# Performance work log

Hardware: AMD Instinct MI355X
Metric: run time of the kernel (lower is better)

## Reference

```python
import jax, jax.numpy as jnp
import numpy as np

L, B, I, H = 256, 16, 2048, 2048
S = R = T = 32  # s_size == t_size is required by the read-hop chaining


def setup_inputs() -> dict:
    key = jax.random.key(0)
    ks = jax.random.split(key, 8)
    def p(k, shape, scale=0.02):
        return jax.random.normal(k, shape, jnp.float32) * scale
    return dict(
        inputs=jax.random.normal(ks[0], (L, B, I), jnp.float32),
        h0=jnp.zeros((B, H), jnp.float32),
        c0=jnp.zeros((B, H), jnp.float32),
        F0=jnp.zeros((B, S * R, T), jnp.float32),
        W_ih=p(ks[1], (4 * H, I)),
        W_hh=p(ks[2], (4 * H, H)),
        b_ih=jnp.zeros((4 * H,), jnp.float32),
        b_hh=jnp.zeros((4 * H,), jnp.float32),
        Ww_w=p(ks[3], (S + R + T + 1, H)),
        Ww_b=jnp.zeros((S + R + T + 1,), jnp.float32),
        Wr_w=p(ks[4], (S + 3 * R, H)),
        Wr_b=jnp.zeros((S + 3 * R,), jnp.float32),
        Wlin_w=p(ks[5], (H, T)),
        Wlin_b=jnp.zeros((H,), jnp.float32),
    )


def _ln(x, eps=1e-5):
    # LayerNorm without affine params (elementwise_affine=False)
    m = jnp.mean(x, -1, keepdims=True)
    v = jnp.var(x, -1, keepdims=True)
    return (x - m) * jax.lax.rsqrt(v + eps)


def reference(inputs, h0, c0, F0, W_ih, W_hh, b_ih, b_hh,
              Ww_w, Ww_b, Wr_w, Wr_b, Wlin_w, Wlin_b):
    # ---- single-layer LSTM (PyTorch gate order i,f,g,o) ----
    bias = b_ih + b_hh
    def lstm_step(carry, x_t):
        h, c = carry
        g = x_t @ W_ih.T + h @ W_hh.T + bias            # [B,4H]
        i, f, gg, o = jnp.split(g, 4, axis=-1)
        c = jax.nn.sigmoid(f) * c + jax.nn.sigmoid(i) * jnp.tanh(gg)
        h = jax.nn.sigmoid(o) * jnp.tanh(c)
        return (h, c), h
    _, x = jax.lax.scan(lstm_step, (h0, c0), inputs)     # x: [L,B,H]

    # ---- Fast Weight Memory: per-step write then 3-hop read ----
    def fwm_step(Fm, x_t):
        # write
        w = x_t @ Ww_w.T + Ww_b                          # [B, S+R+T+1]
        s = jnp.tanh(w[:, :S])
        r = jnp.tanh(w[:, S:S + R])
        t = jnp.tanh(w[:, S + R:S + R + T])
        b = jax.nn.sigmoid(w[:, S + R + T:] + 1.0)       # [B,1]
        sr = (s[:, :, None] * r[:, None, :]).reshape(-1, S * R)   # [B,S*R]
        v = jnp.einsum('bk,bkt->bt', sr, Fm)             # [B,T]
        Fm = Fm + sr[:, :, None] * (b * (t - v))[:, None, :]
        n = jnp.linalg.norm(Fm.reshape(Fm.shape[0], -1), axis=-1)
        Fm = Fm / (jax.nn.relu(n - 1.0) + 1.0)[:, None, None]
        # read (3 hops)
        rv = jnp.tanh(x_t @ Wr_w.T + Wr_b)               # [B, S+3R]
        q = rv[:, :S]
        for j in range(3):
            rj = rv[:, S + j * R:S + (j + 1) * R]
            nr = (q[:, :, None] * rj[:, None, :]).reshape(q.shape[0], -1)
            q = _ln(jnp.einsum('bk,bkt->bt', nr, Fm))    # [B,T]
        return Fm, q

    _, qs = jax.lax.scan(fwm_step, F0, x)                # qs: [L,B,T]
    return x + qs @ Wlin_w.T + Wlin_b                    # [L,B,H]
```

## Files before the change

kernel.cpp:

```cpp
#include <hip/hip_runtime.h>
#include <hip/hip_bf16.h>
#include <cstdint>
#include <cstddef>

#define L_DIM 256
#define B_DIM 16
#define I_DIM 2048
#define H_DIM 2048
#define G4    8192
#define MROWS 4096
#define NWGL  128
#define NPRJ  16
#define NSCN  16

typedef __hip_bfloat16 bf16;
typedef __bf16 bf16x8_t __attribute__((ext_vector_type(8)));
typedef _Float16 f16x8_t __attribute__((ext_vector_type(8)));
typedef _Float16 f16x4_t __attribute__((ext_vector_type(4)));
typedef float f32x4_t   __attribute__((ext_vector_type(4)));

__device__ __forceinline__ bf16 f2b(float f) { return __float2bfloat16(f); }

__device__ __forceinline__ void gl_lds16(const void* g, void* l) {
  __builtin_amdgcn_global_load_lds(
      (const __attribute__((address_space(1))) unsigned int*)g,
      (__attribute__((address_space(3))) unsigned int*)l, 16, 0, 0);
}

__device__ __forceinline__ float sigmoidf_(float x) { return 1.f / (1.f + expf(-x)); }

__device__ __forceinline__ f16x8_t load_f16x8_sc(const _Float16* p) {
  f16x8_t r;
  asm volatile("global_load_dwordx4 %0, %1, off sc0 sc1" : "=v"(r) : "v"(p));
  return r;
}
__device__ __forceinline__ bf16x8_t load_bf16x8_sc(const bf16* p) {
  bf16x8_t r;
  asm volatile("global_load_dwordx4 %0, %1, off sc0 sc1" : "=v"(r) : "v"(p));
  return r;
}
__device__ __forceinline__ float load_f32_sc(const float* p) {
  float r;
  asm volatile("global_load_dword %0, %1, off sc0 sc1" : "=v"(r) : "v"(p));
  return r;
}
__device__ __forceinline__ void store_short_sc(void* p, unsigned int v) {
  asm volatile("global_store_short %0, %1, off sc0 sc1" :: "v"(p), "v"(v) : "memory");
}
__device__ __forceinline__ void store_f32_sc(void* p, float v) {
  asm volatile("global_store_dword %0, %1, off sc0 sc1" :: "v"(p), "v"(v) : "memory");
}

__global__ void prep_kernel(const float* __restrict__ Wih, const float* __restrict__ Whh,
                            const float* __restrict__ inp, const float* __restrict__ Www,
                            const float* __restrict__ Wwb, const float* __restrict__ Wrw,
                            const float* __restrict__ h0,
                            _Float16* __restrict__ Wih_f, _Float16* __restrict__ Whh_f,
                            _Float16* __restrict__ inp_f,
                            bf16* __restrict__ Wq_hi, bf16* __restrict__ Wq_lo,
                            bf16* __restrict__ Wr_hi, bf16* __restrict__ Wr_lo,
                            float* __restrict__ wbpad,
                            _Float16* __restrict__ Xh0)
{
  size_t idx0 = (size_t)blockIdx.x * blockDim.x + threadIdx.x;
  size_t stride = (size_t)gridDim.x * blockDim.x;
  for (size_t i = idx0; i < 16777216ull; i += stride) {
    Wih_f[i] = (_Float16)Wih[i];
    Whh_f[i] = (_Float16)Whh[i];
  }
  for (size_t i = idx0; i < 8388608ull; i += stride) inp_f[i] = (_Float16)inp[i];
  for (size_t i = idx0; i < 262144ull; i += stride) {
    size_t r = i >> 11;
    float q = (r < 97) ? Www[i] : 0.f;
    bf16 qh = f2b(q);
    Wq_hi[i] = qh;
    Wq_lo[i] = f2b(q - (float)qh);
    float rr = Wrw[i];
    bf16 rh = f2b(rr);
    Wr_hi[i] = rh;
    Wr_lo[i] = f2b(rr - (float)rh);
  }
  for (size_t i = idx0; i < 128ull; i += stride) wbpad[i] = (i < 97) ? Wwb[i] : 0.f;
  for (size_t i = idx0; i < 32768ull; i += stride) Xh0[i] = (_Float16)h0[i];
}

__global__ __launch_bounds__(256) void gemm_f16(const _Float16* __restrict__ A,
                                                const _Float16* __restrict__ B,
                                                const float* __restrict__ bih,
                                                const float* __restrict__ bhh,
                                                _Float16* __restrict__ Gin2,
                                                int M, int N, int K)
{
  __shared__ __align__(16) _Float16 As[128 * 32];
  __shared__ __align__(16) _Float16 Bs[128 * 32];
  const int tid  = threadIdx.x;
  const int lane = tid & 63;
  const int w    = tid >> 6;
  const int wm   = w >> 1, wn = w & 1;
  const int m0   = blockIdx.x * 128, n0 = blockIdx.y * 128;

  f32x4_t acc[4][4];
#pragma unroll
  for (int m = 0; m < 4; ++m)
#pragma unroll
    for (int n = 0; n < 4; ++n) acc[m][n] = (f32x4_t){0.f, 0.f, 0.f, 0.f};

  for (int k0 = 0; k0 < K; k0 += 32) {
#pragma unroll
    for (int r = 0; r < 2; ++r) {
      const int base = w * 2048 + r * 1024;
      const int off  = base + lane * 16;
      const int e    = off >> 1;
      const int row  = e >> 5;
      const int col  = e & 31;
      gl_lds16(A + (size_t)(m0 + row) * K + (k0 + col), (char*)As + base);
      gl_lds16(B + (size_t)(n0 + row) * K + (k0 + col), (char*)Bs + base);
    }
    __syncthreads();

    f16x8_t af[4], bfr[4];
    const int kb = (lane >> 4) * 16;
#pragma unroll
    for (int m = 0; m < 4; ++m)
      af[m] = *reinterpret_cast<const f16x8_t*>((const char*)As + (wm * 64 + m * 16 + (lane & 15)) * 64 + kb);
#pragma unroll
    for (int n = 0; n < 4; ++n)
      bfr[n] = *reinterpret_cast<const f16x8_t*>((const char*)Bs + (wn * 64 + n * 16 + (lane & 15)) * 64 + kb);
#pragma unroll
    for (int m = 0; m < 4; ++m)
#pragma unroll
      for (int n = 0; n < 4; ++n)
        acc[m][n] = __builtin_amdgcn_mfma_f32_16x16x32_f16(af[m], bfr[n], acc[m][n], 0, 0, 0);
    __syncthreads();
  }

  const int jj = lane & 15;
#pragma unroll
  for (int n = 0; n < 4; ++n) {
    const int colb = n0 + wn * 64 + n * 16;
    const int gate = colb >> 11;
    const int wg   = (colb & 2047) >> 4;
    const float bv = bih[colb + jj] + bhh[colb + jj];
#pragma unroll
    for (int m = 0; m < 4; ++m) {
      const int rowb = m0 + wm * 64 + m * 16;
      const int t = rowb >> 4;
      f16x4_t v4;
#pragma unroll
      for (int r = 0; r < 4; ++r) v4[r] = (_Float16)(acc[m][n][r] + bv);
      *reinterpret_cast<f16x4_t*>(
          Gin2 + (((size_t)t * NWGL + wg) * 4 + gate) * 256 + jj * 16 + (lane >> 4) * 4) = v4;
    }
  }
}

__global__ __launch_bounds__(512, 2) void fused_rnn(
    const _Float16* __restrict__ Whh,
    const _Float16* __restrict__ Gin2,
    const float* __restrict__ bih, const float* __restrict__ bhh,
    const float* __restrict__ c0,
    const bf16* __restrict__ Wq_hi, const bf16* __restrict__ Wq_lo,
    const bf16* __restrict__ Wr_hi, const bf16* __restrict__ Wr_lo,
    const float* __restrict__ wbpad, const float* __restrict__ Wrb,
    const float* __restrict__ F0,
    _Float16* __restrict__ Xh,
    bf16* __restrict__ XhHi, bf16* __restrict__ XhLo,
    float* __restrict__ Wall, float* __restrict__ RVall,
    _Float16* __restrict__ Gbuf,
    int* lflags, int* pflags)
{
  __shared__ float part[8][4][16][17];
  __shared__ float s_s[32], s_r[32], s_tv[32], s_bb;
  __shared__ float s_rv[128];
  __shared__ float s_v[32];
  __shared__ float s_red[8];

  const int wgid = blockIdx.x;
  const int tid  = threadIdx.x;
  const int lane = tid & 63;
  const int wv   = tid >> 6;

  if (wgid < NWGL) {
    const int wg = wgid;
    const int j0 = wg * 16;
    const int kw = wv * 256;

    f16x8_t whh[4][8];
    {
      const int nn  = lane & 15;
      const int kfo = (lane >> 4) * 8;
#pragma unroll
      for (int g = 0; g < 4; ++g) {
        const size_t grow = (size_t)(g * H_DIM + j0 + nn) * 2048;
#pragma unroll
        for (int ks = 0; ks < 8; ++ks)
          whh[g][ks] = *reinterpret_cast<const f16x8_t*>(Whh + grow + kw + ks * 32 + kfo);
      }
    }

    float c_reg = 0.f, cbr0 = 0.f, cbr1 = 0.f, cbr2 = 0.f, cbr3 = 0.f;
    if (tid < 256) {
      const int bb = tid & 15, jj = tid >> 4;
      const int j = j0 + jj;
      c_reg = c0[bb * H_DIM + j];
      cbr0 = bih[0 * H_DIM + j] + bhh[0 * H_DIM + j];
      cbr1 = bih[1 * H_DIM + j] + bhh[1 * H_DIM + j];
      cbr2 = bih[2 * H_DIM + j] + bhh[2 * H_DIM + j];
      cbr3 = bih[3 * H_DIM + j] + bhh[3 * H_DIM + j];
    }

    const size_t arow = (size_t)(lane & 15) * 2048 + kw + (lane >> 4) * 8;
    const int fidx = ((wv << 4) + (lane & 15)) << 4;

    for (int t = 0; t < L_DIM; ++t) {
      float gin0 = 0.f, gin1 = 0.f, gin2v = 0.f, gin3 = 0.f;
      if (tid < 256) {
        const _Float16* gbase = Gin2 + ((size_t)t * NWGL + wg) * 1024;
        gin0  = (float)gbase[0 * 256 + tid];
        gin1  = (float)gbase[1 * 256 + tid];
        gin2v = (float)gbase[2 * 256 + tid];
        gin3  = (float)gbase[3 * 256 + tid];
      }

      if (t > 0) {
        while (true) {
          const int v = __hip_atomic_load(&lflags[fidx], __ATOMIC_RELAXED,
                                          __HIP_MEMORY_SCOPE_AGENT);
          if (__all(v >= t)) break;
          __builtin_amdgcn_s_sleep(1);
        }
      }

      const size_t hoff = (size_t)t * 32768 + arow;
      f16x8_t hf[8];
#pragma unroll
      for (int ks = 0; ks < 8; ++ks)
        hf[ks] = load_f16x8_sc(Xh + hoff + ks * 32);
      asm volatile("s_waitcnt vmcnt(0)" ::: "memory");
      __builtin_amdgcn_sched_barrier(0);

      f32x4_t acc[4];
#pragma unroll
      for (int g = 0; g < 4; ++g) acc[g] = (f32x4_t){0.f, 0.f, 0.f, 0.f};
#pragma unroll
      for (int ks = 0; ks < 8; ++ks) {
#pragma unroll
        for (int g = 0; g < 4; ++g)
          acc[g] = __builtin_amdgcn_mfma_f32_16x16x32_f16(hf[ks], whh[g][ks], acc[g], 0, 0, 0);
      }
#pragma unroll
      for (int g = 0; g < 4; ++g)
#pragma unroll
        for (int r = 0; r < 4; ++r)
          part[wv][g][(lane >> 4) * 4 + r][lane & 15] = acc[g][r];
      __syncthreads();

      if (tid < 256) {
        const int bb = tid & 15, jj = tid >> 4;
        float g4[4] = {gin0, gin1, gin2v, gin3};
        const float cb4[4] = {cbr0, cbr1, cbr2, cbr3};
#pragma unroll
        for (int g = 0; g < 4; ++g) {
          float s = 0.f;
#pragma unroll
          for (int v = 0; v < 8; ++v) s += part[v][g][bb][jj];
          g4[g] += s + cb4[g];
        }
        const float i_ = sigmoidf_(g4[0]);
        const float f_ = sigmoidf_(g4[1]);
        const float g_ = tanhf(g4[2]);
        const float o_ = sigmoidf_(g4[3]);
        c_reg = f_ * c_reg + i_ * g_;
        const float h = o_ * tanhf(c_reg);
        const int bj = bb * 2048 + j0 + jj;
        const _Float16 hF = (_Float16)h;
        const bf16 hhv = f2b(h);
        const bf16 hlv = f2b(h - (float)hhv);
        const size_t xi = ((size_t)t * 16 + bb) * 2048 + j0 + jj;
        store_short_sc(Xh + (size_t)(t + 1) * 32768 + bj,
                       (unsigned int)__builtin_bit_cast(unsigned short, hF));
        store_short_sc(XhHi + xi,
                       (unsigned int)__builtin_bit_cast(unsigned short, hhv));
        store_short_sc(XhLo + xi,
                       (unsigned int)__builtin_bit_cast(unsigned short, hlv));
      }
      asm volatile("s_waitcnt vmcnt(0)" ::: "memory");
      __syncthreads();

      if (tid == 0)
        __hip_atomic_store(&lflags[wg << 4], t + 1, __ATOMIC_RELAXED,
                           __HIP_MEMORY_SCOPE_AGENT);
    }

  } else if (wgid < NWGL + NPRJ) {
    const int p   = wgid - NWGL;
    const int kw  = wv * 256;
    const int nn  = lane & 15;
    const int kfo = (lane >> 4) * 8;

    bf16x8_t wbh[8], wbl[8];
    {
      const bf16* Bh = (p < 8) ? Wq_hi : Wr_hi;
      const bf16* Bl = (p < 8) ? Wq_lo : Wr_lo;
      const int brow = (p < 8) ? (p * 16 + nn) : ((p - 8) * 16 + nn);
#pragma unroll
      for (int ks = 0; ks < 8; ++ks) {
        const size_t o = (size_t)brow * 2048 + kw + ks * 32 + kfo;
        wbh[ks] = *reinterpret_cast<const bf16x8_t*>(Bh + o);
        wbl[ks] = *reinterpret_cast<const bf16x8_t*>(Bl + o);
      }
    }
    float biasv = 0.f;
    if (tid < 256) {
      const int oo = tid >> 4;
      biasv = (p < 8) ? wbpad[p * 16 + oo] : Wrb[(p - 8) * 16 + oo];
    }

    const size_t axrow = (size_t)(lane & 15) * 2048 + kw + kfo;

    for (int t = 0; t < L_DIM; ++t) {
      while (true) {
        const int v0 = __hip_atomic_load(&lflags[lane << 4], __ATOMIC_RELAXED,
                                         __HIP_MEMORY_SCOPE_AGENT);
        const int v1 = __hip_atomic_load(&lflags[(64 + lane) << 4], __ATOMIC_RELAXED,
                                         __HIP_MEMORY_SCOPE_AGENT);
        if (__all(v0 > t && v1 > t)) break;
        __builtin_amdgcn_s_sleep(1);
      }

      const size_t xoff = (size_t)t * 32768 + axrow;
      bf16x8_t xh[8], xl[8];
#pragma unroll
      for (int ks = 0; ks < 8; ++ks) {
        xh[ks] = load_bf16x8_sc(XhHi + xoff + ks * 32);
        xl[ks] = load_bf16x8_sc(XhLo + xoff + ks * 32);
      }
      asm volatile("s_waitcnt vmcnt(0)" ::: "memory");
      __builtin_amdgcn_sched_barrier(0);

      f32x4_t acc = {0.f, 0.f, 0.f, 0.f};
#pragma unroll
      for (int ks = 0; ks < 8; ++ks) {
        acc = __builtin_amdgcn_mfma_f32_16x16x32_bf16(xh[ks], wbh[ks], acc, 0, 0, 0);
        acc = __builtin_amdgcn_mfma_f32_16x16x32_bf16(xh[ks], wbl[ks], acc, 0, 0, 0);
        acc = __builtin_amdgcn_mfma_f32_16x16x32_bf16(xl[ks], wbh[ks], acc, 0, 0, 0);
      }
#pragma unroll
      for (int r = 0; r < 4; ++r)
        part[wv][0][(lane >> 4) * 4 + r][lane & 15] = acc[r];
      __syncthreads();

      if (tid < 256) {
        const int bb = tid & 15, oo = tid >> 4;
        float s = 0.f;
#pragma unroll
        for (int v = 0; v < 8; ++v) s += part[v][0][bb][oo];
        s += biasv;
        float* dst;
        if (p < 8) {
          dst = Wall + (size_t)(t * 16 + bb) * 128 + p * 16 + oo;
        } else {
          s = tanhf(s);
          dst = RVall + (size_t)(t * 16 + bb) * 128 + (p - 8) * 16 + oo;
        }
        store_f32_sc(dst, s);
      }
      asm volatile("s_waitcnt vmcnt(0)" ::: "memory");
      __syncthreads();

      if (tid == 0)
        __hip_atomic_store(&pflags[p << 4], t + 1, __ATOMIC_RELAXED,
                           __HIP_MEMORY_SCOPE_AGENT);
    }

  } else {
    const int b     = wgid - NWGL - NPRJ;
    const int si    = lane >> 1;
    const int rbase = 16 * (lane & 1);
    const int tl    = lane & 31;

    float F[16][4];
#pragma unroll
    for (int i = 0; i < 16; ++i)
#pragma unroll
      for (int j = 0; j < 4; ++j)
        F[i][j] = F0[((size_t)b * 1024 + (16 * lane + i)) * 32 + 4 * wv + j];

    float N = 0.f;
    {
      float loc = 0.f;
#pragma unroll
      for (int i = 0; i < 16; ++i)
#pragma unroll
        for (int j = 0; j < 4; ++j) loc += F[i][j] * F[i][j];
#pragma unroll
      for (int m = 1; m < 64; m <<= 1) loc += __shfl_xor(loc, m);
      if (lane == 0) s_red[wv] = loc;
      __syncthreads();
#pragma unroll
      for (int k = 0; k < 8; ++k) N += s_red[k];
    }

    for (int t = 0; t < 256; ++t) {
      while (true) {
        const int v = __hip_atomic_load(&pflags[(lane & 15) << 4], __ATOMIC_RELAXED,
                                        __HIP_MEMORY_SCOPE_AGENT);
        if (__all(v > t)) break;
        __builtin_amdgcn_s_sleep(1);
      }

      float wpre = 0.f, rvpre = 0.f;
      if (tid < 97)  wpre = load_f32_sc(Wall + (size_t)(t * 16 + b) * 128 + tid);
      if (tid >= 128 && tid < 256)
        rvpre = load_f32_sc(RVall + (size_t)(t * 16 + b) * 128 + tid - 128);
      asm volatile("s_waitcnt vmcnt(0)" ::: "memory");
      __syncthreads();
      if (tid < 32)       s_s[tid]       = tanhf(wpre);
      else if (tid < 64)  s_r[tid - 32]  = tanhf(wpre);
      else if (tid < 96)  s_tv[tid - 64] = tanhf(wpre);
      else if (tid == 96) s_bb           = sigmoidf_(wpre + 1.f);
      else if (tid >= 128 && tid < 256) s_rv[tid - 128] = rvpre;
      __syncthreads();

      const float sv = s_s[si];
      float sr[16];
#pragma unroll
      for (int i = 0; i < 16; ++i) sr[i] = sv * s_r[rbase + i];

      float vv4[4];
#pragma unroll
      for (int j = 0; j < 4; ++j) {
        float pp = 0.f;
#pragma unroll
        for (int i = 0; i < 16; ++i) pp += sr[i] * F[i][j];
#pragma unroll
        for (int m = 1; m < 64; m <<= 1) pp += __shfl_xor(pp, m);
        vv4[j] = pp;
      }
      if (lane == 0) {
#pragma unroll
        for (int j = 0; j < 4; ++j) s_v[4 * wv + j] = vv4[j];
      }
      __syncthreads();

      const float vt  = s_v[tl];
      const float ut  = s_bb * (s_tv[tl] - vt);
      const float sl  = s_s[tl];
      const float rl  = s_r[tl];
      float uv = ut * vt, uu = ut * ut, ss = sl * sl, rr = rl * rl;
#pragma unroll
      for (int m = 1; m < 32; m <<= 1) {
        uv += __shfl_xor(uv, m);
        uu += __shfl_xor(uu, m);
        ss += __shfl_xor(ss, m);
        rr += __shfl_xor(rr, m);
      }
      const float Np  = N + 2.f * uv + ss * rr * uu;
      const float n_  = sqrtf(Np);
      const float inv = 1.f / (fmaxf(n_ - 1.f, 0.f) + 1.f);
      N = Np * inv * inv;

      float uw[4];
#pragma unroll
      for (int j = 0; j < 4; ++j) uw[j] = __shfl(ut, 4 * wv + j);
#pragma unroll
      for (int i = 0; i < 16; ++i)
#pragma unroll
        for (int j = 0; j < 4; ++j)
          F[i][j] = (F[i][j] + sr[i] * uw[j]) * inv;

      _Float16* gout = Gbuf + ((size_t)(t * 16 + b) * 3) * 1024;
#pragma unroll
      for (int jit = 0; jit < 3; ++jit) {
        float rjv[16];
#pragma unroll
        for (int i = 0; i < 16; ++i) rjv[i] = s_rv[32 + 32 * jit + rbase + i];
        f16x4_t gv;
#pragma unroll
        for (int j = 0; j < 4; ++j) {
          float g = 0.f;
#pragma unroll
          for (int i = 0; i < 16; ++i) g += rjv[i] * F[i][j];
          g += __shfl_xor(g, 1);
          gv[j] = (_Float16)g;
        }
        if ((lane & 1) == 0)
          *reinterpret_cast<f16x4_t*>(gout + jit * 1024 + (lane >> 1) * 32 + 4 * wv) = gv;
      }
    }
  }
}

__global__ __launch_bounds__(256) void qread_out(const _Float16* __restrict__ Gbuf,
                                                 const float* __restrict__ RVall,
                                                 const bf16* __restrict__ Xh1Hi,
                                                 const bf16* __restrict__ Xh1Lo,
                                                 const float* __restrict__ Wlin,
                                                 const float* __restrict__ blin,
                                                 float* __restrict__ out)
{
  __shared__ float qs[32];
  const int row = blockIdx.x;
  const int tid = threadIdx.x;

  if (tid < 64) {
    const int lane  = tid;
    const int tq    = lane & 31;
    const int ihalf = (lane >> 5) * 16;
    const _Float16* G = Gbuf + (size_t)row * 3 * 1024;
    float q = RVall[(size_t)row * 128 + tq];
#pragma unroll 1
    for (int jit = 0; jit < 3; ++jit) {
      float c = 0.f;
#pragma unroll
      for (int i = 0; i < 16; ++i) {
        const float qi = __shfl(q, ihalf + i);
        c += qi * (float)G[jit * 1024 + (ihalf + i) * 32 + tq];
      }
      c += __shfl_xor(c, 32);
      float mval = c;
#pragma unroll
      for (int m = 1; m < 32; m <<= 1) mval += __shfl_xor(mval, m);
      mval *= (1.f / 32.f);
      const float dl = c - mval;
      float var = dl * dl;
#pragma unroll
      for (int m = 1; m < 32; m <<= 1) var += __shfl_xor(var, m);
      var *= (1.f / 32.f);
      q = dl * rsqrtf(var + 1e-5f);
    }
    if (lane < 32) qs[lane] = q;
  }
  __syncthreads();

  for (int h = tid; h < H_DIM; h += 256) {
    const size_t xi = (size_t)row * H_DIM + h;
    float acc = (float)Xh1Hi[xi] + (float)Xh1Lo[xi] + blin[h];
    const float* wr = Wlin + (size_t)h * 32;
#pragma unroll
    for (int t2 = 0; t2 < 32; ++t2) acc += qs[t2] * wr[t2];
    out[xi] = acc;
  }
}

extern "C" void kernel_launch(void* const* d_in, const int* in_sizes, int n_in,
                              void* d_out, int out_size, void* d_ws, size_t ws_size,
                              hipStream_t stream)
{
  (void)in_sizes; (void)n_in; (void)out_size; (void)ws_size;
  const float* inp  = (const float*)d_in[0];
  const float* h0   = (const float*)d_in[1];
  const float* c0   = (const float*)d_in[2];
  const float* F0   = (const float*)d_in[3];
  const float* Wih  = (const float*)d_in[4];
  const float* Whh  = (const float*)d_in[5];
  const float* bih  = (const float*)d_in[6];
  const float* bhh  = (const float*)d_in[7];
  const float* Www  = (const float*)d_in[8];
  const float* Wwb  = (const float*)d_in[9];
  const float* Wrw  = (const float*)d_in[10];
  const float* Wrb  = (const float*)d_in[11];
  const float* Wlin = (const float*)d_in[12];
  const float* blin = (const float*)d_in[13];
  float* out = (float*)d_out;

  char* p = (char*)d_ws;
  auto alloc = [&](size_t bytes) {
    char* r = p;
    p += (bytes + 255) & ~(size_t)255;
    return r;
  };
  _Float16* Whh_f = (_Float16*)alloc(16777216ull * 2);
  _Float16* Wih_f = (_Float16*)alloc(16777216ull * 2);
  _Float16* inp_f = (_Float16*)alloc(8388608ull * 2);
  _Float16* Gin2  = (_Float16*)alloc(33554432ull * 2);
  _Float16* Xh    = (_Float16*)alloc(257ull * 32768 * 2);
  bf16*     XhLo  = (bf16*)alloc(8388608ull * 2);
  bf16*  Wq_hi  = (bf16*)alloc(262144ull * 2);
  bf16*  Wq_lo  = (bf16*)alloc(262144ull * 2);
  bf16*  Wr_hi  = (bf16*)alloc(262144ull * 2);
  bf16*  Wr_lo  = (bf16*)alloc(262144ull * 2);
  float* wbpad  = (float*)alloc(128ull * 4);
  float* Wall   = (float*)alloc(524288ull * 4);
  float* RVall  = (float*)alloc(524288ull * 4);
  _Float16* Gbuf = (_Float16*)alloc(12582912ull * 2);
  int*   flags  = (int*)alloc((NWGL + NPRJ) * 64);
  int*   lflags = flags;
  int*   pflags = flags + NWGL * 16;
  bf16*  XhHi  = (bf16*)inp_f;

  prep_kernel<<<2048, 256, 0, stream>>>(Wih, Whh, inp, Www, Wwb, Wrw, h0,
                                        Wih_f, Whh_f, inp_f,
                                        Wq_hi, Wq_lo, Wr_hi, Wr_lo, wbpad, Xh);

  gemm_f16<<<dim3(32, 64), 256, 0, stream>>>(inp_f, Wih_f, bih, bhh, Gin2,
                                             MROWS, G4, 2048);

  hipMemsetAsync(flags, 0, (NWGL + NPRJ) * 64, stream);
  {
    void* kargs[] = {
      (void*)&Whh_f, (void*)&Gin2, (void*)&bih, (void*)&bhh, (void*)&c0,
      (void*)&Wq_hi, (void*)&Wq_lo, (void*)&Wr_hi, (void*)&Wr_lo,
      (void*)&wbpad, (void*)&Wrb, (void*)&F0,
      (void*)&Xh, (void*)&XhHi, (void*)&XhLo,
      (void*)&Wall, (void*)&RVall, (void*)&Gbuf,
      (void*)&lflags, (void*)&pflags
    };
    hipLaunchCooperativeKernel((const void*)fused_rnn,
                               dim3(NWGL + NPRJ + NSCN), dim3(512),
                               kargs, 0, stream);
  }

  qread_out<<<4096, 256, 0, stream>>>(Gbuf, RVall, XhHi, XhLo, Wlin, blin, out);
}
```

Before: 1.870 ms.

## Fuse input projection into recurrent LSTM kernel, dropping separate input GEMM

Removes the standalone input-projection GEMM and its Gin2 buffer. Each recurrent workgroup now computes x_t·W_ih for its gate slice with MFMA before waiting on the step flag, so this work can overlap the inter-workgroup synchronisation latency. The trade-off is that W_ih is reloaded from global memory every timestep (it does not fit in registers alongside W_hh), which adds heavy per-step bandwidth on the serial critical path. XhHi gets its own allocation instead of aliasing inp_f, since inp_f is now read during the recurrence.

```diff
diff --git a/kernel.cpp b/kernel.cpp
--- a/kernel.cpp
+++ b/kernel.cpp
@@ -20,12 +20,6 @@
 typedef float f32x4_t   __attribute__((ext_vector_type(4)));
 
 __device__ __forceinline__ bf16 f2b(float f) { return __float2bfloat16(f); }
-
-__device__ __forceinline__ void gl_lds16(const void* g, void* l) {
-  __builtin_amdgcn_global_load_lds(
-      (const __attribute__((address_space(1))) unsigned int*)g,
-      (__attribute__((address_space(3))) unsigned int*)l, 16, 0, 0);
-}
 
 __device__ __forceinline__ float sigmoidf_(float x) { return 1.f / (1.f + expf(-x)); }
 
@@ -84,79 +78,10 @@
   for (size_t i = idx0; i < 32768ull; i += stride) Xh0[i] = (_Float16)h0[i];
 }
 
-__global__ __launch_bounds__(256) void gemm_f16(const _Float16* __restrict__ A,
-                                                const _Float16* __restrict__ B,
-                                                const float* __restrict__ bih,
-                                                const float* __restrict__ bhh,
-                                                _Float16* __restrict__ Gin2,
-                                                int M, int N, int K)
-{
-  __shared__ __align__(16) _Float16 As[128 * 32];
-  __shared__ __align__(16) _Float16 Bs[128 * 32];
-  const int tid  = threadIdx.x;
-  const int lane = tid & 63;
-  const int w    = tid >> 6;
-  const int wm   = w >> 1, wn = w & 1;
-  const int m0   = blockIdx.x * 128, n0 = blockIdx.y * 128;
-
-  f32x4_t acc[4][4];
-#pragma unroll
-  for (int m = 0; m < 4; ++m)
-#pragma unroll
-    for (int n = 0; n < 4; ++n) acc[m][n] = (f32x4_t){0.f, 0.f, 0.f, 0.f};
-
-  for (int k0 = 0; k0 < K; k0 += 32) {
-#pragma unroll
-    for (int r = 0; r < 2; ++r) {
-      const int base = w * 2048 + r * 1024;
-      const int off  = base + lane * 16;
-      const int e    = off >> 1;
-      const int row  = e >> 5;
-      const int col  = e & 31;
-      gl_lds16(A + (size_t)(m0 + row) * K + (k0 + col), (char*)As + base);
-      gl_lds16(B + (size_t)(n0 + row) * K + (k0 + col), (char*)Bs + base);
-    }
-    __syncthreads();
-
-    f16x8_t af[4], bfr[4];
-    const int kb = (lane >> 4) * 16;
-#pragma unroll
-    for (int m = 0; m < 4; ++m)
-      af[m] = *reinterpret_cast<const f16x8_t*>((const char*)As + (wm * 64 + m * 16 + (lane & 15)) * 64 + kb);
-#pragma unroll
-    for (int n = 0; n < 4; ++n)
-      bfr[n] = *reinterpret_cast<const f16x8_t*>((const char*)Bs + (wn * 64 + n * 16 + (lane & 15)) * 64 + kb);
-#pragma unroll
-    for (int m = 0; m < 4; ++m)
-#pragma unroll
-      for (int n = 0; n < 4; ++n)
-        acc[m][n] = __builtin_amdgcn_mfma_f32_16x16x32_f16(af[m], bfr[n], acc[m][n], 0, 0, 0);
-    __syncthreads();
-  }
-
-  const int jj = lane & 15;
-#pragma unroll
-  for (int n = 0; n < 4; ++n) {
-    const int colb = n0 + wn * 64 + n * 16;
-    const int gate = colb >> 11;
-    const int wg   = (colb & 2047) >> 4;
-    const float bv = bih[colb + jj] + bhh[colb + jj];
-#pragma unroll
-    for (int m = 0; m < 4; ++m) {
-      const int rowb = m0 + wm * 64 + m * 16;
-      const int t = rowb >> 4;
-      f16x4_t v4;
-#pragma unroll
-      for (int r = 0; r < 4; ++r) v4[r] = (_Float16)(acc[m][n][r] + bv);
-      *reinterpret_cast<f16x4_t*>(
-          Gin2 + (((size_t)t * NWGL + wg) * 4 + gate) * 256 + jj * 16 + (lane >> 4) * 4) = v4;
-    }
-  }
-}
-
 __global__ __launch_bounds__(512, 2) void fused_rnn(
     const _Float16* __restrict__ Whh,
-    const _Float16* __restrict__ Gin2,
+    const _Float16* __restrict__ Wih_f,
+    const _Float16* __restrict__ inp_f,
     const float* __restrict__ bih, const float* __restrict__ bhh,
     const float* __restrict__ c0,
     const bf16* __restrict__ Wq_hi, const bf16* __restrict__ Wq_lo,
@@ -184,11 +109,11 @@
     const int wg = wgid;
     const int j0 = wg * 16;
     const int kw = wv * 256;
+    const int nn  = lane & 15;
+    const int kfo = (lane >> 4) * 8;
 
     f16x8_t whh[4][8];
     {
-      const int nn  = lane & 15;
-      const int kfo = (lane >> 4) * 8;
 #pragma unroll
       for (int g = 0; g < 4; ++g) {
         const size_t grow = (size_t)(g * H_DIM + j0 + nn) * 2048;
@@ -213,13 +138,24 @@
     const int fidx = ((wv << 4) + (lane & 15)) << 4;
 
     for (int t = 0; t < L_DIM; ++t) {
-      float gin0 = 0.f, gin1 = 0.f, gin2v = 0.f, gin3 = 0.f;
-      if (tid < 256) {
-        const _Float16* gbase = Gin2 + ((size_t)t * NWGL + wg) * 1024;
-        gin0  = (float)gbase[0 * 256 + tid];
-        gin1  = (float)gbase[1 * 256 + tid];
-        gin2v = (float)gbase[2 * 256 + tid];
-        gin3  = (float)gbase[3 * 256 + tid];
+      f32x4_t acc[4];
+#pragma unroll
+      for (int g = 0; g < 4; ++g) acc[g] = (f32x4_t){0.f, 0.f, 0.f, 0.f};
+      {
+        const size_t xoff = (size_t)t * 32768 + arow;
+        f16x8_t xf[8];
+#pragma unroll
+        for (int ks = 0; ks < 8; ++ks)
+          xf[ks] = *reinterpret_cast<const f16x8_t*>(inp_f + xoff + ks * 32);
+#pragma unroll
+        for (int g = 0; g < 4; ++g) {
+          const size_t grow = (size_t)(g * H_DIM + j0 + nn) * 2048;
+#pragma unroll
+          for (int ks = 0; ks < 8; ++ks) {
+            f16x8_t wb = *reinterpret_cast<const f16x8_t*>(Wih_f + grow + kw + ks * 32 + kfo);
+            acc[g] = __builtin_amdgcn_mfma_f32_16x16x32_f16(xf[ks], wb, acc[g], 0, 0, 0);
+          }
+        }
       }
 
       if (t > 0) {
@@ -239,9 +175,6 @@
       asm volatile("s_waitcnt vmcnt(0)" ::: "memory");
       __builtin_amdgcn_sched_barrier(0);
 
-      f32x4_t acc[4];
-#pragma unroll
-      for (int g = 0; g < 4; ++g) acc[g] = (f32x4_t){0.f, 0.f, 0.f, 0.f};
 #pragma unroll
       for (int ks = 0; ks < 8; ++ks) {
 #pragma unroll
@@ -257,14 +190,14 @@
 
       if (tid < 256) {
         const int bb = tid & 15, jj = tid >> 4;
-        float g4[4] = {gin0, gin1, gin2v, gin3};
+        float g4[4];
         const float cb4[4] = {cbr0, cbr1, cbr2, cbr3};
 #pragma unroll
         for (int g = 0; g < 4; ++g) {
           float s = 0.f;
 #pragma unroll
           for (int v = 0; v < 8; ++v) s += part[v][g][bb][jj];
-          g4[g] += s + cb4[g];
+          g4[g] = s + cb4[g];
         }
         const float i_ = sigmoidf_(g4[0]);
         const float f_ = sigmoidf_(g4[1]);
@@ -573,8 +506,8 @@
   _Float16* Whh_f = (_Float16*)alloc(16777216ull * 2);
   _Float16* Wih_f = (_Float16*)alloc(16777216ull * 2);
   _Float16* inp_f = (_Float16*)alloc(8388608ull * 2);
-  _Float16* Gin2  = (_Float16*)alloc(33554432ull * 2);
   _Float16* Xh    = (_Float16*)alloc(257ull * 32768 * 2);
+  bf16*     XhHi  = (bf16*)alloc(8388608ull * 2);
   bf16*     XhLo  = (bf16*)alloc(8388608ull * 2);
   bf16*  Wq_hi  = (bf16*)alloc(262144ull * 2);
   bf16*  Wq_lo  = (bf16*)alloc(262144ull * 2);
@@ -587,19 +520,16 @@
   int*   flags  = (int*)alloc((NWGL + NPRJ) * 64);
   int*   lflags = flags;
   int*   pflags = flags + NWGL * 16;
-  bf16*  XhHi  = (bf16*)inp_f;
 
   prep_kernel<<<2048, 256, 0, stream>>>(Wih, Whh, inp, Www, Wwb, Wrw, h0,
                                         Wih_f, Whh_f, inp_f,
                                         Wq_hi, Wq_lo, Wr_hi, Wr_lo, wbpad, Xh);
 
-  gemm_f16<<<dim3(32, 64), 256, 0, stream>>>(inp_f, Wih_f, bih, bhh, Gin2,
-                                             MROWS, G4, 2048);
-
   hipMemsetAsync(flags, 0, (NWGL + NPRJ) * 64, stream);
   {
     void* kargs[] = {
-      (void*)&Whh_f, (void*)&Gin2, (void*)&bih, (void*)&bhh, (void*)&c0,
+      (void*)&Whh_f, (void*)&Wih_f, (void*)&inp_f,
+      (void*)&bih, (void*)&bhh, (void*)&c0,
       (void*)&Wq_hi, (void*)&Wq_lo, (void*)&Wr_hi, (void*)&Wr_lo,
       (void*)&wbpad, (void*)&Wrb, (void*)&F0,
       (void*)&Xh, (void*)&XhHi, (void*)&XhLo,
```

Measured after the change: 2.914 ms. +55.8%, slower.
